# Kernel optimization log

Measured on AMD Instinct MI355X. Metric: run time of the kernel, lower is better.

Reference implementation:

```python
import jax, jax.numpy as jnp
import numpy as np

BETA = 0.9
THRESHOLD = 1.0
NUM_STEPS = 100

# Heaviside spike with snntorch-default ATan surrogate gradient (alpha=2):
# forward: 1[u > 0]; backward: g / (1 + (pi*u)^2)
@jax.custom_vjp
def spike(u):
    return (u > 0).astype(u.dtype)

def _spike_fwd(u):
    return (u > 0).astype(u.dtype), u

def _spike_bwd(u, g):
    return (g / (1.0 + (jnp.pi * u) ** 2),)

spike.defvjp(_spike_fwd, _spike_bwd)


def setup_inputs() -> dict:
    key = jax.random.key(0)
    ks = jax.random.split(key, 8)
    B, D_IN, H, D_OUT = 256, 1024, 2048, 1024
    def lin(k, fan_out, fan_in):
        bound = 1.0 / np.sqrt(fan_in)
        kw, kb = jax.random.split(k)
        W = jax.random.uniform(kw, (fan_out, fan_in), jnp.float32, -bound, bound)
        b = jax.random.uniform(kb, (fan_out,), jnp.float32, -bound, bound)
        return W, b
    W0, b0 = lin(ks[0], H, D_IN)
    W1, b1 = lin(ks[1], H, H)
    W2, b2 = lin(ks[2], D_OUT, H)
    x = jax.random.normal(ks[3], (B, D_IN), jnp.float32)
    return {"x": x, "W0": W0, "b0": b0, "W1": W1, "b1": b1, "W2": W2, "b2": b2}


def _lif(cur, mem_prev):
    # snntorch Leaky, reset_mechanism='subtract': reset computed from previous
    # state (detached), then mem update, then fire.
    reset = jax.lax.stop_gradient((mem_prev > THRESHOLD).astype(cur.dtype))
    mem_new = BETA * mem_prev + cur - reset * THRESHOLD
    spk = spike(mem_new - THRESHOLD)
    # NOTE: the source module does `mem[i], spk[i] = layer(cur, mem[i])` while
    # snn.Leaky returns (spk, mem) -- i.e. the outputs are SWAPPED. We reproduce
    # that faithfully: the stored 'mem' state is the spike, and the stored 'spk'
    # (fed to the next layer / emitted as output) is the membrane potential.
    return spk, mem_new


def reference(x, W0, b0, W1, b1, W2, b2):
    B = x.shape[0]
    m_init = (jnp.zeros((B, W0.shape[0]), x.dtype),
              jnp.zeros((B, W1.shape[0]), x.dtype),
              jnp.zeros((B, W2.shape[0]), x.dtype))

    cur0 = x @ W0.T + b0  # input is constant across steps; hoist the GEMM

    def step(mems, _):
        m0_spk, s0_mem = _lif(cur0, mems[0])
        cur1 = s0_mem @ W1.T + b1          # 'spk[0]' in source is actually mem
        m1_spk, s1_mem = _lif(cur1, mems[1])
        cur2 = s1_mem @ W2.T + b2          # 'spk[-2]' = layer-1 'spk' (= mem)
        m2_spk, s2_mem = _lif(cur2, mems[2])
        return (m0_spk, m1_spk, m2_spk), s2_mem

    _, outs = jax.lax.scan(step, m_init, None, length=NUM_STEPS)
    return outs  # [num_steps, batch, output_size]
```

## Files before the change

### kernel.cpp

```cpp
#include <hip/hip_runtime.h>


typedef unsigned short ushort_t;
typedef __attribute__((ext_vector_type(8))) short bf16x8;
typedef __attribute__((ext_vector_type(4))) float f32x4;

#define SDELTA 1.0e-3f
#define NS 12
#define NS2 6

__device__ inline ushort_t f2bf(float f) {
    unsigned u = __float_as_uint(f);
    u += 0x7FFFu + ((u >> 16) & 1u);
    return (ushort_t)(u >> 16);
}
__device__ inline float bf2f(ushort_t h) { return __uint_as_float((unsigned)h << 16); }
__device__ inline float4 ld4(const float* p) { return *reinterpret_cast<const float4*>(p); }

__device__ inline void gload16(const void* g, void* l) {
    __builtin_amdgcn_global_load_lds(
        (__attribute__((address_space(1))) void*)g,
        (__attribute__((address_space(3))) void*)l, 16, 0, 0);
}

__device__ inline void do_split(const float4* src, ushort_t* dst, int i, int logK)
{
    float4 v = src[i];
    const int K = 1 << logK;
    const int e0 = i * 4;
    const int r = e0 >> logK, k = e0 & (K - 1);
    ushort_t* row = dst + (size_t)r * 2 * K;
    ushort4 h, l;
    h.x = f2bf(v.x); l.x = f2bf(v.x - bf2f(h.x));
    h.y = f2bf(v.y); l.y = f2bf(v.y - bf2f(h.y));
    h.z = f2bf(v.z); l.z = f2bf(v.z - bf2f(h.z));
    h.w = f2bf(v.w); l.w = f2bf(v.w - bf2f(h.w));
    *reinterpret_cast<ushort4*>(row + k) = h;
    *reinterpret_cast<ushort4*>(row + K + k) = l;
}

__device__ __attribute__((always_inline)) inline void gemm_body(
    const ushort_t* __restrict__ A, const ushort_t* __restrict__ W,
    float* __restrict__ P, int M, int N, int K, int Kc, int nx, int ny,
    int lin, int nwg, ushort_t* As, ushort_t* Ws)
{
    const int swzb = (lin & 7) * (nwg >> 3) + (lin >> 3);
    const int nxy = nx * ny;
    const int bz  = swzb / nxy;
    const int rem = swzb - bz * nxy;
    const int by  = rem / nx;
    const int bx  = rem - by * nx;

    const int tid  = threadIdx.x;
    const int lane = tid & 63;
    const int wid  = tid >> 6;
    const int row0 = by * 128;
    const int col0 = bx * 128;
    const int k0   = bz * Kc;
    const int st   = 2 * K;
    const int aoff = (k0 < K) ? k0 : (k0 - K);
    const int woff = (k0 < 2 * K) ? k0 : (k0 - 2 * K);

    const int srow = wid * 32 + (lane >> 3);
    const int scol = (((lane & 7) ^ ((lane >> 3) & 7))) * 8;
    const ushort_t* Ag = A + (size_t)(row0 + srow) * st + aoff + scol;
    const ushort_t* Wg = W + (size_t)(col0 + srow) * st + woff + scol;

    const int wr = wid >> 1, wc = wid & 1;
    const int l15 = lane & 15;
    const int kh  = lane >> 4;
    const int swz8 = l15 & 7;
    const int ch0 = ((kh + 0) ^ swz8) * 8;
    const int ch1 = ((kh + 4) ^ swz8) * 8;
    int aRow[4], bRow[4];
#pragma unroll
    for (int m = 0; m < 4; ++m) aRow[m] = (wr * 64 + m * 16 + l15) * 64;
#pragma unroll
    for (int n = 0; n < 4; ++n) bRow[n] = (wc * 64 + n * 16 + l15) * 64;

    f32x4 acc[4][4] = {};
    const int NIT = Kc / 64;

    for (int it = 0; it < NIT; ++it) {
        const int kk = it * 64;
#pragma unroll
        for (int i = 0; i < 4; ++i) {
            gload16(Ag + (size_t)(i * 8) * st + kk, &As[(wid * 32 + i * 8) * 64]);
            gload16(Wg + (size_t)(i * 8) * st + kk, &Ws[(wid * 32 + i * 8) * 64]);
        }
        __syncthreads();
#pragma unroll
        for (int ks = 0; ks < 2; ++ks) {
            const int ch = ks ? ch1 : ch0;
            bf16x8 af[4], bf[4];
#pragma unroll
            for (int m = 0; m < 4; ++m)
                af[m] = *reinterpret_cast<const bf16x8*>(&As[aRow[m] + ch]);
#pragma unroll
            for (int n = 0; n < 4; ++n)
                bf[n] = *reinterpret_cast<const bf16x8*>(&Ws[bRow[n] + ch]);
#pragma unroll
            for (int m = 0; m < 4; ++m)
#pragma unroll
                for (int n = 0; n < 4; ++n)
                    acc[m][n] = __builtin_amdgcn_mfma_f32_16x16x32_bf16(
                        af[m], bf[n], acc[m][n], 0, 0, 0);
        }
        __syncthreads();
    }

    float* Pp = P + ((size_t)bz * M + row0) * N + col0;
#pragma unroll
    for (int n = 0; n < 4; ++n) {
        const int col = wc * 64 + n * 16 + l15;
#pragma unroll
        for (int m = 0; m < 4; ++m) {
            const int rb = wr * 64 + m * 16 + kh * 4;
#pragma unroll
            for (int i = 0; i < 4; ++i)
                Pp[(size_t)(rb + i) * N + col] = acc[m][n][i];
        }
    }
}

__global__ __launch_bounds__(256) void gemm_splitk(
    const ushort_t* __restrict__ A, const ushort_t* __restrict__ W,
    float* __restrict__ P, int M, int N, int K, int Kc, int nx, int ny)
{
    __shared__ ushort_t As[128 * 64];
    __shared__ ushort_t Ws[128 * 64];
    gemm_body(A, W, P, M, N, K, Kc, nx, ny, blockIdx.x, gridDim.x, As, Ws);
}

__global__ __launch_bounds__(256) void gemm0_cvt12(
    const ushort_t* __restrict__ xb, const ushort_t* __restrict__ Wb0,
    float* __restrict__ P,
    const float4* __restrict__ W1, const float4* __restrict__ W2,
    ushort_t* __restrict__ Wb1, ushort_t* __restrict__ Wb2)
{
    __shared__ ushort_t As[128 * 64];
    __shared__ ushort_t Ws[128 * 64];
    const int b = blockIdx.x;
    if (b < 384) {
        gemm_body(xb, Wb0, P, 256, 2048, 1024, 256, 16, 2, b, 384, As, Ws);
    } else if (b < 384 + 4096) {
        do_split(W1, Wb1, (b - 384) * 256 + threadIdx.x, 11);
    } else {
        do_split(W2, Wb2, (b - 4480) * 256 + threadIdx.x, 11);
    }
}

__global__ __launch_bounds__(256) void cvt_xw0(
    const float4* __restrict__ x, const float4* __restrict__ W0,
    ushort_t* __restrict__ xb, ushort_t* __restrict__ Wb0)
{
    const int b = blockIdx.x, tid = threadIdx.x;
    if (b < 256) do_split(x,  xb,  b * 256 + tid, 10);
    else         do_split(W0, Wb0, (b - 256) * 256 + tid, 10);
}

__device__ inline int flag4(float4 v, int e0, int* loc, int lc)
{
    float vv[4] = {v.x, v.y, v.z, v.w};
#pragma unroll
    for (int c = 0; c < 4; ++c)
        if ((fabsf(vv[c] - 1.0f) < SDELTA) || (fabsf(vv[c] - 0.1f) < SDELTA))
            loc[lc++] = e0 + c;
    return lc;
}

__device__ inline void wsplit2(ushort_t* row, int k, float4 v)
{
    ushort4 h, l;
    h.x = f2bf(v.x); l.x = f2bf(v.x - bf2f(h.x));
    h.y = f2bf(v.y); l.y = f2bf(v.y - bf2f(h.y));
    h.z = f2bf(v.z); l.z = f2bf(v.z - bf2f(h.z));
    h.w = f2bf(v.w); l.w = f2bf(v.w - bf2f(h.w));
    *reinterpret_cast<ushort4*>(row + k) = h;
    *reinterpret_cast<ushort4*>(row + 2048 + k) = l;
}

__device__ inline void patch2(ushort_t* row, int c, float v)
{
    ushort_t h = f2bf(v);
    ushort_t l = f2bf(v - bf2f(h));
    row[c] = h; row[2048 + c] = l;
}

__device__ inline float4 lifstep(float4 cur, float4 gate)
{
    float4 o;
    o.x = cur.x + ((gate.x > 1.0f) ? 0.9f : 0.0f);
    o.y = cur.y + ((gate.y > 1.0f) ? 0.9f : 0.0f);
    o.z = cur.z + ((gate.z > 1.0f) ? 0.9f : 0.0f);
    o.w = cur.w + ((gate.w > 1.0f) ? 0.9f : 0.0f);
    return o;
}

__device__ inline double wred(double p)
{
#pragma unroll
    for (int off = 32; off; off >>= 1) p += __shfl_down(p, off);
    return __shfl(p, 0);
}

__global__ __launch_bounds__(256) void fused0(
    const float4* __restrict__ P, const float* __restrict__ bias,
    float* __restrict__ C0f, ushort_t* __restrict__ A1b,
    const float* __restrict__ X, const float* __restrict__ W0,
    const float* __restrict__ b0f)
{
    __shared__ int flist[1024];
    __shared__ int fcnt;
    if (threadIdx.x == 0) fcnt = 0;
    __syncthreads();

    const int i = blockIdx.x * 256 + threadIdx.x;
    float4 s = P[i];
#pragma unroll
    for (int j = 1; j < NS; ++j) {
        float4 t = P[(size_t)j * 131072 + i];
        s.x += t.x; s.y += t.y; s.z += t.z; s.w += t.w;
    }
    const float4 bv = *reinterpret_cast<const float4*>(bias + ((i * 4) & 2047));
    s.x += bv.x; s.y += bv.y; s.z += bv.z; s.w += bv.w;
    reinterpret_cast<float4*>(C0f)[i] = s;
    int loc[4];
    int lc = flag4(s, i * 4, loc, 0);
    for (int j = 0; j < lc; ++j) { int p = atomicAdd(&fcnt, 1); flist[p] = loc[j]; }
    float4 mi = lifstep(s, s);
    const int e0 = i * 4, r = e0 >> 11, k = e0 & 2047;
    wsplit2(A1b + (size_t)r * 4096, k, s);
    wsplit2(A1b + (size_t)(256 + r) * 4096, k, mi);
    __syncthreads();

    const int lane = threadIdx.x & 63;
    const int wid  = threadIdx.x >> 6;
    for (int e = wid; e < fcnt; e += 4) {
        const int idx = flist[e];
        const int rr = idx >> 11, cc = idx & 2047;
        double p = 0.0;
        for (int kk = lane * 4; kk < 1024; kk += 256) {
            float4 a4 = ld4(X + (size_t)rr * 1024 + kk);
            float4 w4 = ld4(W0 + (size_t)cc * 1024 + kk);
            p = fma((double)a4.x, (double)w4.x, p);
            p = fma((double)a4.y, (double)w4.y, p);
            p = fma((double)a4.z, (double)w4.z, p);
            p = fma((double)a4.w, (double)w4.w, p);
        }
        const double tot = wred(p);
        if (lane == 0) {
            float c = (float)(tot + (double)b0f[cc]);
            C0f[idx] = c;
            float mi2 = c + ((c > 1.0f) ? 0.9f : 0.0f);
            patch2(A1b + (size_t)rr * 4096, cc, c);
            patch2(A1b + (size_t)(256 + rr) * 4096, cc, mi2);
        }
    }
}

__global__ __launch_bounds__(256) void fused1(
    const float4* __restrict__ P, const float* __restrict__ bias,
    float* __restrict__ C1f, ushort_t* __restrict__ A2b,
    const float* __restrict__ C0, const float* __restrict__ W1)
{
    __shared__ int flist[2048];
    __shared__ int fcnt;
    if (threadIdx.x == 0) fcnt = 0;
    __syncthreads();

    const int i = blockIdx.x * 256 + threadIdx.x;
    float4* C1 = reinterpret_cast<float4*>(C1f);
    float4 c0 = P[i];
    float4 ci = P[131072 + i];
#pragma unroll
    for (int j = 1; j < NS; ++j) {
        float4 t0 = P[(size_t)j * 262144 + i];
        float4 t1 = P[(size_t)j * 262144 + 131072 + i];
        c0.x += t0.x; c0.y += t0.y; c0.z += t0.z; c0.w += t0.w;
        ci.x += t1.x; ci.y += t1.y; ci.z += t1.z; ci.w += t1.w;
    }
    const float4 bv = *reinterpret_cast<const float4*>(bias + ((i * 4) & 2047));
    c0.x += bv.x; c0.y += bv.y; c0.z += bv.z; c0.w += bv.w;
    ci.x += bv.x; ci.y += bv.y; ci.z += bv.z; ci.w += bv.w;
    C1[i] = c0;
    C1[131072 + i] = ci;
    int loc[8];
    int lc = flag4(c0, i * 4, loc, 0);
    lc = flag4(ci, (131072 + i) * 4, loc, lc);
    for (int j = 0; j < lc; ++j) { int p = atomicAdd(&fcnt, 1); flist[p] = loc[j]; }
    float4 m1 = lifstep(ci, c0);
    float4 m2 = lifstep(ci, m1);
    const int e0 = i * 4, r = e0 >> 11, k = e0 & 2047;
    wsplit2(A2b + (size_t)r * 4096, k, c0);
    wsplit2(A2b + (size_t)(256 + r) * 4096, k, m1);
    wsplit2(A2b + (size_t)(512 + r) * 4096, k, m2);
    __syncthreads();

    const int lane = threadIdx.x & 63;
    const int wid  = threadIdx.x >> 6;
    for (int e = wid; e < fcnt; e += 4) {
        const int idx = flist[e];
        const int cc = idx & 2047;
        const int rp = (idx >> 11) & 255;
        double p0 = 0.0, p1 = 0.0;
        for (int kk = lane * 4; kk < 2048; kk += 256) {
            float4 a4 = ld4(C0 + (size_t)rp * 2048 + kk);
            float4 w4 = ld4(W1 + (size_t)cc * 2048 + kk);
            float4 b4 = lifstep(a4, a4);
            p0 = fma((double)a4.x, (double)w4.x, p0);
            p0 = fma((double)a4.y, (double)w4.y, p0);
            p0 = fma((double)a4.z, (double)w4.z, p0);
            p0 = fma((double)a4.w, (double)w4.w, p0);
            p1 = fma((double)b4.x, (double)w4.x, p1);
            p1 = fma((double)b4.y, (double)w4.y, p1);
            p1 = fma((double)b4.z, (double)w4.z, p1);
            p1 = fma((double)b4.w, (double)w4.w, p1);
        }
        const double t0 = wred(p0);
        const double t1 = wred(p1);
        if (lane == 0) {
            float fc0 = (float)(t0 + (double)bias[cc]);
            float fci = (float)(t1 + (double)bias[cc]);
            C1f[(size_t)rp * 2048 + cc] = fc0;
            C1f[(size_t)(256 + rp) * 2048 + cc] = fci;
            float m1s = fci + ((fc0 > 1.0f) ? 0.9f : 0.0f);
            float m2s = fci + ((m1s > 1.0f) ? 0.9f : 0.0f);
            patch2(A2b + (size_t)rp * 4096, cc, fc0);
            patch2(A2b + (size_t)(256 + rp) * 4096, cc, m1s);
            patch2(A2b + (size_t)(512 + rp) * 4096, cc, m2s);
        }
    }
}

__global__ __launch_bounds__(256) void fused2_bcast(
    const float4* __restrict__ P, const float* __restrict__ bias,
    float* __restrict__ C2f, const float* __restrict__ C1,
    const float* __restrict__ W2, float4* __restrict__ out)
{
    __shared__ int flist[3072];
    __shared__ int fcnt;
    if (threadIdx.x == 0) fcnt = 0;
    __syncthreads();

    const int i = blockIdx.x * 256 + threadIdx.x;
    float4* C2 = reinterpret_cast<float4*>(C2f);
    const float4 bv = *reinterpret_cast<const float4*>(bias + ((i * 4) & 1023));
#pragma unroll
    for (int v = 0; v < 3; ++v) {
        float4 s = P[(size_t)v * 65536 + i];
#pragma unroll
        for (int j = 1; j < NS2; ++j) {
            float4 t = P[(size_t)j * 196608 + (size_t)v * 65536 + i];
            s.x += t.x; s.y += t.y; s.z += t.z; s.w += t.w;
        }
        s.x += bv.x; s.y += bv.y; s.z += bv.z; s.w += bv.w;
        C2[(size_t)v * 65536 + i] = s;
        int loc[4];
        int lc = flag4(s, (v * 65536 + i) * 4, loc, 0);
        for (int j = 0; j < lc; ++j) { int p = atomicAdd(&fcnt, 1); flist[p] = loc[j]; }
    }
    __syncthreads();

    const int lane = threadIdx.x & 63;
    const int wid  = threadIdx.x >> 6;
    for (int e = wid; e < fcnt; e += 4) {
        const int idx = flist[e];
        const int cc = idx & 1023;
        const int rp = (idx >> 10) & 255;
        double pA = 0.0, pB = 0.0, pC = 0.0;
        for (int kk = lane * 4; kk < 2048; kk += 256) {
            float4 c04 = ld4(C1 + (size_t)rp * 2048 + kk);
            float4 ci4 = ld4(C1 + (size_t)(256 + rp) * 2048 + kk);
            float4 w4  = ld4(W2 + (size_t)cc * 2048 + kk);
            float4 m14 = lifstep(ci4, c04);
            float4 m24 = lifstep(ci4, m14);
            pA = fma((double)c04.x, (double)w4.x, pA);
            pA = fma((double)c04.y, (double)w4.y, pA);
            pA = fma((double)c04.z, (double)w4.z, pA);
            pA = fma((double)c04.w, (double)w4.w, pA);
            pB = fma((double)m14.x, (double)w4.x, pB);
            pB = fma((double)m14.y, (double)w4.y, pB);
            pB = fma((double)m14.z, (double)w4.z, pB);
            pB = fma((double)m14.w, (double)w4.w, pB);
            pC = fma((double)m24.x, (double)w4.x, pC);
            pC = fma((double)m24.y, (double)w4.y, pC);
            pC = fma((double)m24.z, (double)w4.z, pC);
            pC = fma((double)m24.w, (double)w4.w, pC);
        }
        const double tA = wred(pA);
        const double tB = wred(pB);
        const double tC = wred(pC);
        if (lane == 0) {
            C2f[(size_t)rp * 1024 + cc]         = (float)(tA + (double)bias[cc]);
            C2f[(size_t)(256 + rp) * 1024 + cc] = (float)(tB + (double)bias[cc]);
            C2f[(size_t)(512 + rp) * 1024 + cc] = (float)(tC + (double)bias[cc]);
        }
    }
    __syncthreads();

    float4 c0 = C2[i];
    float4 c1 = C2[65536 + i];
    float4 ci = C2[131072 + i];
    float4 m0 = c0;
    float4 m1 = lifstep(c1, m0);
    float4 m2 = lifstep(ci, m1);
    float4 m3 = lifstep(ci, m2);
    out[i] = m0;
    out[65536 + i] = m1;
    out[131072 + i] = m2;
    for (int t = 3; t < 80; ++t)
        out[(size_t)t * 65536 + i] = m3;
}

__global__ __launch_bounds__(256) void tail_bcast(const float4* __restrict__ c2,
                                                  float4* __restrict__ out)
{
    const int i = blockIdx.x * 256 + threadIdx.x;
    float4 c0 = c2[i], c1 = c2[65536 + i], ci = c2[131072 + i];
    float4 m1 = lifstep(c1, c0);
    float4 m2 = lifstep(ci, m1);
    float4 m3 = lifstep(ci, m2);
    const int t0 = 80 + blockIdx.y * 4;
#pragma unroll
    for (int j = 0; j < 4; ++j)
        out[(size_t)(t0 + j) * 65536 + i] = m3;
}

extern "C" void kernel_launch(void* const* d_in, const int* in_sizes, int n_in,
                              void* d_out, int out_size, void* d_ws, size_t ws_size,
                              hipStream_t stream)
{
    const float* x  = (const float*)d_in[0];
    const float* W0 = (const float*)d_in[1];
    const float* b0 = (const float*)d_in[2];
    const float* W1 = (const float*)d_in[3];
    const float* b1 = (const float*)d_in[4];
    const float* W2 = (const float*)d_in[5];
    const float* b2 = (const float*)d_in[6];
    float* out = (float*)d_out;
    float* ws  = (float*)d_ws;

    float* C0 = ws;
    float* C1 = ws + 524288;
    float* C2 = ws + 1572864;

    ushort_t* Wb0 = (ushort_t*)(out);
    ushort_t* Wb1 = (ushort_t*)(out + 2097152);
    ushort_t* Wb2 = (ushort_t*)(out + 6291456);
    ushort_t* xb  = (ushort_t*)(out + 8388608);
    ushort_t* A1b = (ushort_t*)(out + 8650752);
    ushort_t* A2b = (ushort_t*)(out + 9699328);
    float* Pbuf   = out + 11272192;
    float* Pbuf2  = out + 20971520;

    dim3 blk(256);

    cvt_xw0<<<dim3(2304), blk, 0, stream>>>((const float4*)x, (const float4*)W0,
                                            xb, Wb0);

    gemm0_cvt12<<<dim3(6528), blk, 0, stream>>>(xb, Wb0, Pbuf,
                                                (const float4*)W1, (const float4*)W2,
                                                Wb1, Wb2);
    fused0<<<dim3(512), blk, 0, stream>>>((const float4*)Pbuf, b0, C0,
                                          A1b, x, W0, b0);

    gemm_splitk<<<dim3(768), blk, 0, stream>>>(A1b, Wb1, Pbuf, 512, 2048, 2048, 512, 16, 4);
    fused1<<<dim3(512), blk, 0, stream>>>((const float4*)Pbuf, b1, C1,
                                          A2b, C0, W1);

    gemm_splitk<<<dim3(288), blk, 0, stream>>>(A2b, Wb2, Pbuf2, 768, 1024, 2048, 1024, 8, 6);
    fused2_bcast<<<dim3(256), blk, 0, stream>>>((const float4*)Pbuf2, b2, C2, C1, W2,
                                                (float4*)out);
    tail_bcast<<<dim3(256, 5), blk, 0, stream>>>((const float4*)C2, (float4*)out);
}
```

Measured before the change: 142.8 us.

## Fuse split-K GEMMs with their epilogue kernels via a software grid barrier

```diff
diff --git a/kernel.cpp b/kernel.cpp
--- a/kernel.cpp
+++ b/kernel.cpp
@@ -21,6 +21,25 @@
     __builtin_amdgcn_global_load_lds(
         (__attribute__((address_space(1))) void*)g,
         (__attribute__((address_space(3))) void*)l, 16, 0, 0);
+}
+
+__device__ inline void gridbar(int* bar, int nblk)
+{
+    __syncthreads();
+    if (threadIdx.x == 0) {
+        int* cnt = bar;
+        int* gen = bar + 8;
+        int g = __hip_atomic_load(gen, __ATOMIC_RELAXED, __HIP_MEMORY_SCOPE_AGENT);
+        int a = __hip_atomic_fetch_add(cnt, 1, __ATOMIC_ACQ_REL, __HIP_MEMORY_SCOPE_AGENT);
+        if (a == nblk - 1) {
+            __hip_atomic_store(cnt, 0, __ATOMIC_RELAXED, __HIP_MEMORY_SCOPE_AGENT);
+            __hip_atomic_store(gen, g + 1, __ATOMIC_RELEASE, __HIP_MEMORY_SCOPE_AGENT);
+        } else {
+            while (__hip_atomic_load(gen, __ATOMIC_ACQUIRE, __HIP_MEMORY_SCOPE_AGENT) == g)
+                __builtin_amdgcn_s_sleep(2);
+        }
+    }
+    __syncthreads();
 }
 
 __device__ inline void do_split(const float4* src, ushort_t* dst, int i, int logK)
@@ -121,15 +140,6 @@
                 Pp[(size_t)(rb + i) * N + col] = acc[m][n][i];
         }
     }
-}
-
-__global__ __launch_bounds__(256) void gemm_splitk(
-    const ushort_t* __restrict__ A, const ushort_t* __restrict__ W,
-    float* __restrict__ P, int M, int N, int K, int Kc, int nx, int ny)
-{
-    __shared__ ushort_t As[128 * 64];
-    __shared__ ushort_t Ws[128 * 64];
-    gemm_body(A, W, P, M, N, K, Kc, nx, ny, blockIdx.x, gridDim.x, As, Ws);
 }
 
 __global__ __launch_bounds__(256) void gemm0_cvt12(
@@ -259,42 +269,54 @@
     }
 }
 
-__global__ __launch_bounds__(256) void fused1(
-    const float4* __restrict__ P, const float* __restrict__ bias,
+__global__ void __launch_bounds__(256, 3) gemm1_fused1(
+    const ushort_t* __restrict__ A1b, const ushort_t* __restrict__ Wb1,
+    float* __restrict__ P, const float* __restrict__ bias,
     float* __restrict__ C1f, ushort_t* __restrict__ A2b,
-    const float* __restrict__ C0, const float* __restrict__ W1)
-{
-    __shared__ int flist[2048];
+    const float* __restrict__ C0, const float* __restrict__ W1,
+    int* __restrict__ bar)
+{
+    __shared__ ushort_t As[128 * 64];
+    __shared__ ushort_t Ws[128 * 64];
     __shared__ int fcnt;
+
+    gemm_body(A1b, Wb1, P, 512, 2048, 2048, 512, 16, 4, blockIdx.x, 768, As, Ws);
+    gridbar(bar, 768);
+
+    int* flist = (int*)As;
     if (threadIdx.x == 0) fcnt = 0;
     __syncthreads();
 
     const int i = blockIdx.x * 256 + threadIdx.x;
-    float4* C1 = reinterpret_cast<float4*>(C1f);
-    float4 c0 = P[i];
-    float4 ci = P[131072 + i];
-#pragma unroll
-    for (int j = 1; j < NS; ++j) {
-        float4 t0 = P[(size_t)j * 262144 + i];
-        float4 t1 = P[(size_t)j * 262144 + 131072 + i];
-        c0.x += t0.x; c0.y += t0.y; c0.z += t0.z; c0.w += t0.w;
-        ci.x += t1.x; ci.y += t1.y; ci.z += t1.z; ci.w += t1.w;
-    }
-    const float4 bv = *reinterpret_cast<const float4*>(bias + ((i * 4) & 2047));
-    c0.x += bv.x; c0.y += bv.y; c0.z += bv.z; c0.w += bv.w;
-    ci.x += bv.x; ci.y += bv.y; ci.z += bv.z; ci.w += bv.w;
-    C1[i] = c0;
-    C1[131072 + i] = ci;
-    int loc[8];
-    int lc = flag4(c0, i * 4, loc, 0);
-    lc = flag4(ci, (131072 + i) * 4, loc, lc);
-    for (int j = 0; j < lc; ++j) { int p = atomicAdd(&fcnt, 1); flist[p] = loc[j]; }
-    float4 m1 = lifstep(ci, c0);
-    float4 m2 = lifstep(ci, m1);
-    const int e0 = i * 4, r = e0 >> 11, k = e0 & 2047;
-    wsplit2(A2b + (size_t)r * 4096, k, c0);
-    wsplit2(A2b + (size_t)(256 + r) * 4096, k, m1);
-    wsplit2(A2b + (size_t)(512 + r) * 4096, k, m2);
+    const bool act = (i < 131072);
+    if (act) {
+        float4* C1 = reinterpret_cast<float4*>(C1f);
+        const float4* P4 = (const float4*)P;
+        float4 c0 = P4[i];
+        float4 ci = P4[131072 + i];
+#pragma unroll
+        for (int j = 1; j < NS; ++j) {
+            float4 t0 = P4[(size_t)j * 262144 + i];
+            float4 t1 = P4[(size_t)j * 262144 + 131072 + i];
+            c0.x += t0.x; c0.y += t0.y; c0.z += t0.z; c0.w += t0.w;
+            ci.x += t1.x; ci.y += t1.y; ci.z += t1.z; ci.w += t1.w;
+        }
+        const float4 bv = *reinterpret_cast<const float4*>(bias + ((i * 4) & 2047));
+        c0.x += bv.x; c0.y += bv.y; c0.z += bv.z; c0.w += bv.w;
+        ci.x += bv.x; ci.y += bv.y; ci.z += bv.z; ci.w += bv.w;
+        C1[i] = c0;
+        C1[131072 + i] = ci;
+        int loc[8];
+        int lc = flag4(c0, i * 4, loc, 0);
+        lc = flag4(ci, (131072 + i) * 4, loc, lc);
+        for (int j = 0; j < lc; ++j) { int p = atomicAdd(&fcnt, 1); flist[p] = loc[j]; }
+        float4 m1 = lifstep(ci, c0);
+        float4 m2 = lifstep(ci, m1);
+        const int e0 = i * 4, r = e0 >> 11, k = e0 & 2047;
+        wsplit2(A2b + (size_t)r * 4096, k, c0);
+        wsplit2(A2b + (size_t)(256 + r) * 4096, k, m1);
+        wsplit2(A2b + (size_t)(512 + r) * 4096, k, m2);
+    }
     __syncthreads();
 
     const int lane = threadIdx.x & 63;
@@ -333,32 +355,44 @@
     }
 }
 
-__global__ __launch_bounds__(256) void fused2_bcast(
-    const float4* __restrict__ P, const float* __restrict__ bias,
+__global__ void __launch_bounds__(256, 3) gemm2_fused2b(
+    const ushort_t* __restrict__ A2b, const ushort_t* __restrict__ Wb2,
+    float* __restrict__ P, const float* __restrict__ bias,
     float* __restrict__ C2f, const float* __restrict__ C1,
-    const float* __restrict__ W2, float4* __restrict__ out)
-{
-    __shared__ int flist[3072];
+    const float* __restrict__ W2, float4* __restrict__ out,
+    int* __restrict__ bar)
+{
+    __shared__ ushort_t As[128 * 64];
+    __shared__ ushort_t Ws[128 * 64];
     __shared__ int fcnt;
+
+    gemm_body(A2b, Wb2, P, 768, 1024, 2048, 1024, 8, 6, blockIdx.x, 288, As, Ws);
+    gridbar(bar, 288);
+
+    int* flist = (int*)As;
     if (threadIdx.x == 0) fcnt = 0;
     __syncthreads();
 
     const int i = blockIdx.x * 256 + threadIdx.x;
+    const bool act = (i < 65536);
     float4* C2 = reinterpret_cast<float4*>(C2f);
-    const float4 bv = *reinterpret_cast<const float4*>(bias + ((i * 4) & 1023));
-#pragma unroll
-    for (int v = 0; v < 3; ++v) {
-        float4 s = P[(size_t)v * 65536 + i];
-#pragma unroll
-        for (int j = 1; j < NS2; ++j) {
-            float4 t = P[(size_t)j * 196608 + (size_t)v * 65536 + i];
-            s.x += t.x; s.y += t.y; s.z += t.z; s.w += t.w;
-        }
-        s.x += bv.x; s.y += bv.y; s.z += bv.z; s.w += bv.w;
-        C2[(size_t)v * 65536 + i] = s;
-        int loc[4];
-        int lc = flag4(s, (v * 65536 + i) * 4, loc, 0);
-        for (int j = 0; j < lc; ++j) { int p = atomicAdd(&fcnt, 1); flist[p] = loc[j]; }
+    const float4* P4 = (const float4*)P;
+    if (act) {
+        const float4 bv = *reinterpret_cast<const float4*>(bias + ((i * 4) & 1023));
+#pragma unroll
+        for (int v = 0; v < 3; ++v) {
+            float4 s = P4[(size_t)v * 65536 + i];
+#pragma unroll
+            for (int j = 1; j < NS2; ++j) {
+                float4 t = P4[(size_t)j * 196608 + (size_t)v * 65536 + i];
+                s.x += t.x; s.y += t.y; s.z += t.z; s.w += t.w;
+            }
+            s.x += bv.x; s.y += bv.y; s.z += bv.z; s.w += bv.w;
+            C2[(size_t)v * 65536 + i] = s;
+            int loc[4];
+            int lc = flag4(s, (v * 65536 + i) * 4, loc, 0);
+            for (int j = 0; j < lc; ++j) { int p = atomicAdd(&fcnt, 1); flist[p] = loc[j]; }
+        }
     }
     __syncthreads();
 
@@ -399,18 +433,20 @@
     }
     __syncthreads();
 
-    float4 c0 = C2[i];
-    float4 c1 = C2[65536 + i];
-    float4 ci = C2[131072 + i];
-    float4 m0 = c0;
-    float4 m1 = lifstep(c1, m0);
-    float4 m2 = lifstep(ci, m1);
-    float4 m3 = lifstep(ci, m2);
-    out[i] = m0;
-    out[65536 + i] = m1;
-    out[131072 + i] = m2;
-    for (int t = 3; t < 80; ++t)
-        out[(size_t)t * 65536 + i] = m3;
+    if (act) {
+        float4 c0 = C2[i];
+        float4 c1 = C2[65536 + i];
+        float4 ci = C2[131072 + i];
+        float4 m0 = c0;
+        float4 m1 = lifstep(c1, m0);
+        float4 m2 = lifstep(ci, m1);
+        float4 m3 = lifstep(ci, m2);
+        out[i] = m0;
+        out[65536 + i] = m1;
+        out[131072 + i] = m2;
+        for (int t = 3; t < 80; ++t)
+            out[(size_t)t * 65536 + i] = m3;
+    }
 }
 
 __global__ __launch_bounds__(256) void tail_bcast(const float4* __restrict__ c2,
@@ -444,6 +480,8 @@
     float* C0 = ws;
     float* C1 = ws + 524288;
     float* C2 = ws + 1572864;
+    int* bar1 = (int*)(ws + 2359296);
+    int* bar2 = bar1 + 16;
 
     ushort_t* Wb0 = (ushort_t*)(out);
     ushort_t* Wb1 = (ushort_t*)(out + 2097152);
@@ -456,6 +494,8 @@
 
     dim3 blk(256);
 
+    hipMemsetAsync((void*)bar1, 0, 128, stream);
+
     cvt_xw0<<<dim3(2304), blk, 0, stream>>>((const float4*)x, (const float4*)W0,
                                             xb, Wb0);
 
@@ -465,12 +505,11 @@
     fused0<<<dim3(512), blk, 0, stream>>>((const float4*)Pbuf, b0, C0,
                                           A1b, x, W0, b0);
 
-    gemm_splitk<<<dim3(768), blk, 0, stream>>>(A1b, Wb1, Pbuf, 512, 2048, 2048, 512, 16, 4);
-    fused1<<<dim3(512), blk, 0, stream>>>((const float4*)Pbuf, b1, C1,
-                                          A2b, C0, W1);
-
-    gemm_splitk<<<dim3(288), blk, 0, stream>>>(A2b, Wb2, Pbuf2, 768, 1024, 2048, 1024, 8, 6);
-    fused2_bcast<<<dim3(256), blk, 0, stream>>>((const float4*)Pbuf2, b2, C2, C1, W2,
-                                                (float4*)out);
+    gemm1_fused1<<<dim3(768), blk, 0, stream>>>(A1b, Wb1, Pbuf, b1, C1,
+                                                A2b, C0, W1, bar1);
+
+    gemm2_fused2b<<<dim3(288), blk, 0, stream>>>(A2b, Wb2, Pbuf2, b2, C2, C1, W2,
+                                                 (float4*)out, bar2);
+
     tail_bcast<<<dim3(256, 5), blk, 0, stream>>>((const float4*)C2, (float4*)out);
 }
```

Result: slower. 310.8 us (+117.6%).
